# Performance work log

Hardware: AMD Instinct MI355X
Metric: run time of the kernel (lower is better)

The kernel has to match this reference:

```python
import jax, jax.numpy as jnp
import numpy as np

S_LEN, BATCH, HID, HEADS = 2048, 4, 1024, 16
HD = HID // HEADS


def setup_inputs() -> dict:
    key = jax.random.key(0)
    ks = jax.random.split(key, 6)

    def lin_w(k, out_dim, in_dim):
        return jax.random.normal(k, (out_dim, in_dim), jnp.float32) * (1.0 / np.sqrt(in_dim))

    return {
        "hidden_states": jax.random.normal(ks[0], (S_LEN, BATCH, HID), jnp.float32),
        "Wq": lin_w(ks[1], HID, HID), "bq": jnp.zeros((HID,), jnp.float32),
        "Wk": lin_w(ks[2], HID, HID), "bk": jnp.zeros((HID,), jnp.float32),
        "Wv": lin_w(ks[3], HID, HID), "bv": jnp.zeros((HID,), jnp.float32),
        "Wf": lin_w(ks[4], HEADS, HID), "bf": jnp.zeros((HEADS,), jnp.float32),
        "Wo": lin_w(ks[5], HID, HID), "bo": jnp.zeros((HID,), jnp.float32),
    }


def _forget_attention(hidden_states, Wq, bq, Wk, bk, Wv, bv, Wf, bf, Wo, bo):
    S, B, H = hidden_states.shape
    nh, hd = HEADS, HD

    def shape(x):
        return x.reshape(S, B, nh, hd)

    q = shape(hidden_states @ Wq.T + bq)
    k = shape(hidden_states @ Wk.T + bk)
    v = shape(hidden_states @ Wv.T + bv)

    # kernel_fn = elu(x) + 1
    phi_q = jax.nn.elu(q) + 1.0
    phi_k = jax.nn.elu(k) + 1.0

    f = jax.nn.sigmoid(hidden_states @ Wf.T + bf)  # [S, B, nh]

    # F_{t,j} = prod_{i=j+1}^{t} f_i  factorizes into the recurrence:
    #   S_t = f_t * S_{t-1} + phi_k_t (x) v_t ;  z_t = f_t * z_{t-1} + phi_k_t
    # out_t = (phi_q_t . S_t) / (phi_q_t . z_t + eps)
    def step(carry, xs):
        Sm, z = carry                      # [B,nh,hd,hd], [B,nh,hd]
        ft, pk, pq, vt = xs                # [B,nh], [B,nh,hd] x3
        fte = ft[..., None]
        Sm = fte[..., None] * Sm + pk[..., :, None] * vt[..., None, :]
        z = fte * z + pk
        num = jnp.einsum('bhd,bhde->bhe', pq, Sm)
        den = jnp.einsum('bhd,bhd->bh', pq, z)[..., None]
        return (Sm, z), num / (den + 1e-6)

    init = (jnp.zeros((B, nh, hd, hd), hidden_states.dtype),
            jnp.zeros((B, nh, hd), hidden_states.dtype))
    _, out = jax.lax.scan(step, init, (f, phi_k, phi_q, v))

    out = out.reshape(S, B, H) @ Wo.T + bo
    return out, f


def reference(hidden_states, Wq, bq, Wk, bk, Wv, bv, Wf, bf, Wo, bo):
    out, f = _forget_attention(hidden_states, Wq, bq, Wk, bk, Wv, bv, Wf, bf, Wo, bo)
    return (out, jnp.zeros_like(out), f)
```

## Files before the change

### kernel.cpp

```cpp
#include <hip/hip_runtime.h>
#include <hip/hip_bf16.h>
#include <math.h>

#define S_LEN 2048
#define BATCH 4
#define HID   1024
#define HEADS 16
#define HD    64
#define SB    (S_LEN*BATCH)
#define CHUNK 64
#define NCHUNK (S_LEN/CHUNK)
#define BH    (BATCH*HEADS)
#define NSTK  3200

typedef __bf16 bf16x8 __attribute__((ext_vector_type(8)));
typedef float  f32x4  __attribute__((ext_vector_type(4)));
typedef unsigned short ushort_t;
typedef unsigned short u16x8 __attribute__((ext_vector_type(8)));

__device__ __forceinline__ unsigned short f2bf(float x) {
    union { float f; unsigned int u; } un; un.f = x;
    unsigned int u = un.u;
    unsigned int r = (u + 0x7FFFu + ((u >> 16) & 1u)) >> 16;
    return (unsigned short)r;
}
__device__ __forceinline__ float bf2f(unsigned short s) {
    union { unsigned int u; float f; } un; un.u = ((unsigned int)s) << 16;
    return un.f;
}

#define NXU (SB*HID/4)
#define NW1 (NSTK*HID/4)
#define NW2 (HID*HID/4)
#define NBU (NSTK/4)
#define NTOT (NXU+NW1+NW2+NBU)

__global__ __launch_bounds__(256) void prep_kernel(
    const float* __restrict__ X,  const float* __restrict__ Wq,
    const float* __restrict__ Wk, const float* __restrict__ Wv,
    const float* __restrict__ Wf, const float* __restrict__ Wo,
    const float* __restrict__ bq, const float* __restrict__ bk,
    const float* __restrict__ bv, const float* __restrict__ bf,
    ushort_t* __restrict__ Xb, ushort_t* __restrict__ Wstk,
    ushort_t* __restrict__ Wob, float* __restrict__ bstk)
{
    const int i = blockIdx.x * 256 + threadIdx.x;
    if (i < NXU) {
        float4 v = ((const float4*)X)[i];
        ushort4 o; o.x=f2bf(v.x); o.y=f2bf(v.y); o.z=f2bf(v.z); o.w=f2bf(v.w);
        ((ushort4*)Xb)[i] = o;
    } else if (i < NXU + NW1) {
        const int idx4 = (i - NXU) * 4;
        const int row = idx4 >> 10, col = idx4 & 1023;
        float4 v;
        if      (row < 1024) v = *(const float4*)(Wq + (size_t)row*HID + col);
        else if (row < 2048) v = *(const float4*)(Wk + (size_t)(row-1024)*HID + col);
        else if (row < 3072) v = *(const float4*)(Wv + (size_t)(row-2048)*HID + col);
        else if (row < 3088) v = *(const float4*)(Wf + (size_t)(row-3072)*HID + col);
        else                 v = make_float4(0.f,0.f,0.f,0.f);
        ushort4 o; o.x=f2bf(v.x); o.y=f2bf(v.y); o.z=f2bf(v.z); o.w=f2bf(v.w);
        *(ushort4*)(Wstk + idx4) = o;
    } else if (i < NXU + NW1 + NW2) {
        const int idx4 = (i - NXU - NW1) * 4;
        float4 v = *(const float4*)(Wo + idx4);
        ushort4 o; o.x=f2bf(v.x); o.y=f2bf(v.y); o.z=f2bf(v.z); o.w=f2bf(v.w);
        *(ushort4*)(Wob + idx4) = o;
    } else if (i < NTOT) {
        const int idx4 = (i - NXU - NW1 - NW2) * 4;
        #pragma unroll
        for (int t = 0; t < 4; ++t) {
            const int c = idx4 + t;
            float v;
            if      (c < 1024) v = bq[c];
            else if (c < 2048) v = bk[c-1024];
            else if (c < 3072) v = bv[c-2048];
            else if (c < 3088) v = bf[c-3072];
            else               v = 0.f;
            bstk[c] = v;
        }
    }
}

__global__ __launch_bounds__(256) void qkvf_gemm(
    const ushort_t* __restrict__ X, const ushort_t* __restrict__ W,
    const float* __restrict__ bias,
    ushort_t* __restrict__ Q, ushort_t* __restrict__ Kr,
    ushort_t* __restrict__ V,
    float* __restrict__ f_out, float* __restrict__ logf_out)
{
    __shared__ ushort_t As[128 * 32];
    __shared__ ushort_t Bs[128 * 32];

    const int tid  = threadIdx.x;
    const int wave = tid >> 6, lane = tid & 63;
    const int waveM = wave >> 1, waveN = wave & 1;
    const int rowBase = blockIdx.x * 128;
    const int colBase = blockIdx.y * 128;
    const int K = HID;

    f32x4 acc[4][4];
    #pragma unroll
    for (int i = 0; i < 4; ++i)
        #pragma unroll
        for (int j = 0; j < 4; ++j)
            acc[i][j] = (f32x4){0.f, 0.f, 0.f, 0.f};

    const int srow = lane >> 2;
    const int scol = (lane & 3) * 8;

    const ushort_t* gA0 = X + (size_t)(rowBase + wave*16 + srow) * K + scol;
    const ushort_t* gB0 = W + (size_t)(colBase + wave*16 + srow) * K + scol;
    ushort_t* lA = As + (wave*16)*32;
    ushort_t* lB = Bs + (wave*16)*32;

    const int fr = lane & 15;
    const int fk = (lane >> 4) * 8;

    for (int k0 = 0; k0 < K; k0 += 32) {
        __builtin_amdgcn_global_load_lds(
            (const __attribute__((address_space(1))) void*)(gA0 + k0),
            (__attribute__((address_space(3))) void*)lA, 16, 0, 0);
        __builtin_amdgcn_global_load_lds(
            (const __attribute__((address_space(1))) void*)(gA0 + (size_t)64*K + k0),
            (__attribute__((address_space(3))) void*)(lA + 64*32), 16, 0, 0);
        __builtin_amdgcn_global_load_lds(
            (const __attribute__((address_space(1))) void*)(gB0 + k0),
            (__attribute__((address_space(3))) void*)lB, 16, 0, 0);
        __builtin_amdgcn_global_load_lds(
            (const __attribute__((address_space(1))) void*)(gB0 + (size_t)64*K + k0),
            (__attribute__((address_space(3))) void*)(lB + 64*32), 16, 0, 0);

        __syncthreads();

        bf16x8 a[4], b[4];
        #pragma unroll
        for (int i = 0; i < 4; ++i)
            a[i] = *(const bf16x8*)(As + (waveM*64 + i*16 + fr)*32 + fk);
        #pragma unroll
        for (int j = 0; j < 4; ++j)
            b[j] = *(const bf16x8*)(Bs + (waveN*64 + j*16 + fr)*32 + fk);

        #pragma unroll
        for (int i = 0; i < 4; ++i)
            #pragma unroll
            for (int j = 0; j < 4; ++j)
                acc[i][j] = __builtin_amdgcn_mfma_f32_16x16x32_bf16(
                    a[i], b[j], acc[i][j], 0, 0, 0);

        __syncthreads();
    }

    const int er = (lane >> 4) * 4;
    const int ec = lane & 15;
    #pragma unroll
    for (int i = 0; i < 4; ++i) {
        #pragma unroll
        for (int j = 0; j < 4; ++j) {
            const int r0 = rowBase + waveM*64 + i*16 + er;
            const int c0 = colBase + waveN*64 + j*16;
            if (c0 >= 3088) continue;
            const int c  = c0 + ec;
            const float bv = bias[c];
            #pragma unroll
            for (int k = 0; k < 4; ++k) {
                float v = acc[i][j][k] + bv;
                const int r = r0 + k;
                if (c0 < 1024) {
                    v = (v > 0.f) ? (v + 1.f) : __expf(v);
                    Q[(size_t)r * HID + c] = f2bf(v);
                } else if (c0 < 2048) {
                    v = (v > 0.f) ? (v + 1.f) : __expf(v);
                    Kr[(size_t)r * HID + (c - 1024)] = f2bf(v);
                } else if (c0 < 3072) {
                    V[(size_t)r * HID + (c - 2048)] = f2bf(v);
                } else {
                    const int n = c - 3072;
                    const float fv = 1.f / (1.f + __expf(-v));
                    f_out[(size_t)r * HEADS + n]    = fv;
                    logf_out[(size_t)r * HEADS + n] = -__logf(1.f + __expf(-v));
                }
            }
        }
    }
}

__global__ __launch_bounds__(256) void gemm_out(
    const ushort_t* __restrict__ X, const ushort_t* __restrict__ W,
    const float* __restrict__ bias, float* __restrict__ Y,
    float* __restrict__ Yzero)
{
    __shared__ ushort_t As[128 * 32];
    __shared__ ushort_t Bs[128 * 32];

    const int tid  = threadIdx.x;
    const int wave = tid >> 6, lane = tid & 63;
    const int waveM = wave >> 1, waveN = wave & 1;
    const int rowBase = blockIdx.x * 128;
    const int colBase = blockIdx.y * 128;
    const int K = HID, N = HID;

    f32x4 acc[4][4];
    #pragma unroll
    for (int i = 0; i < 4; ++i)
        #pragma unroll
        for (int j = 0; j < 4; ++j)
            acc[i][j] = (f32x4){0.f, 0.f, 0.f, 0.f};

    const int srow = lane >> 2;
    const int scol = (lane & 3) * 8;

    const ushort_t* gA0 = X + (size_t)(rowBase + wave*16 + srow) * K + scol;
    const ushort_t* gB0 = W + (size_t)(colBase + wave*16 + srow) * K + scol;
    ushort_t* lA = As + (wave*16)*32;
    ushort_t* lB = Bs + (wave*16)*32;

    const int fr = lane & 15;
    const int fk = (lane >> 4) * 8;

    for (int k0 = 0; k0 < K; k0 += 32) {
        __builtin_amdgcn_global_load_lds(
            (const __attribute__((address_space(1))) void*)(gA0 + k0),
            (__attribute__((address_space(3))) void*)lA, 16, 0, 0);
        __builtin_amdgcn_global_load_lds(
            (const __attribute__((address_space(1))) void*)(gA0 + (size_t)64*K + k0),
            (__attribute__((address_space(3))) void*)(lA + 64*32), 16, 0, 0);
        __builtin_amdgcn_global_load_lds(
            (const __attribute__((address_space(1))) void*)(gB0 + k0),
            (__attribute__((address_space(3))) void*)lB, 16, 0, 0);
        __builtin_amdgcn_global_load_lds(
            (const __attribute__((address_space(1))) void*)(gB0 + (size_t)64*K + k0),
            (__attribute__((address_space(3))) void*)(lB + 64*32), 16, 0, 0);

        __syncthreads();

        bf16x8 a[4], b[4];
        #pragma unroll
        for (int i = 0; i < 4; ++i)
            a[i] = *(const bf16x8*)(As + (waveM*64 + i*16 + fr)*32 + fk);
        #pragma unroll
        for (int j = 0; j < 4; ++j)
            b[j] = *(const bf16x8*)(Bs + (waveN*64 + j*16 + fr)*32 + fk);

        #pragma unroll
        for (int i = 0; i < 4; ++i)
            #pragma unroll
            for (int j = 0; j < 4; ++j)
                acc[i][j] = __builtin_amdgcn_mfma_f32_16x16x32_bf16(
                    a[i], b[j], acc[i][j], 0, 0, 0);

        __syncthreads();
    }

    const int er = (lane >> 4) * 4;
    const int ec = lane & 15;
    #pragma unroll
    for (int i = 0; i < 4; ++i) {
        #pragma unroll
        for (int j = 0; j < 4; ++j) {
            const int r0 = rowBase + waveM*64 + i*16 + er;
            const int c  = colBase + waveN*64 + j*16 + ec;
            const float bv = bias[c];
            #pragma unroll
            for (int k = 0; k < 4; ++k) {
                const size_t off = (size_t)(r0 + k) * N + c;
                Y[off] = acc[i][j][k] + bv;
                Yzero[off] = 0.f;
            }
        }
    }
}

__global__ __launch_bounds__(256) void pass1_kernel(
    const ushort_t* __restrict__ Kp, const ushort_t* __restrict__ Vp,
    const float* __restrict__ logf,
    float* __restrict__ Schunk, float* __restrict__ zchunk,
    float* __restrict__ Dchunk)
{
    __shared__ __align__(16) char smem[18688];
    ushort_t* vsT = (ushort_t*)smem;
    ushort_t* kTd = (ushort_t*)(smem + 9216);
    float*    exd = (float*)(smem + 18432);

    const int chunk = blockIdx.x;
    const int bh = blockIdx.y;
    const int b = bh >> 4, h = bh & 15;
    const int tid = threadIdx.x;
    const int wv = tid >> 6, ln = tid & 63;
    const int fr = ln & 15, q4 = ln >> 4;
    const size_t slot = (size_t)bh * NCHUNK + chunk;

    u16x8 vreg[2], kreg[2];
    #pragma unroll
    for (int it = 0; it < 2; ++it) {
        const int u = it*256 + tid;
        const int j = u >> 3, d8 = (u & 7) * 8;
        const size_t base = (size_t)((chunk*64 + j)*BATCH + b)*HID + h*HD + d8;
        vreg[it] = *(const u16x8*)(Vp + base);
        kreg[it] = *(const u16x8*)(Kp + base);
    }
    if (tid < 64) {
        float v = logf[(size_t)((chunk*64 + tid)*BATCH + b) * HEADS + h];
        #pragma unroll
        for (int off = 1; off < 64; off <<= 1) {
            float n = __shfl_up(v, off);
            if (tid >= off) v += n;
        }
        const float tot = __shfl(v, 63);
        exd[tid] = __expf(tot - v);
        if (tid == 63) Dchunk[slot] = __expf(tot);
    }
    __syncthreads();

    #pragma unroll
    for (int it = 0; it < 2; ++it) {
        const int u = it*256 + tid;
        const int j = u >> 3, d8 = (u & 7) * 8;
        const float ex = exd[j];
        #pragma unroll
        for (int i = 0; i < 8; ++i) {
            vsT[(d8+i)*72 + j] = vreg[it][i];
            kTd[(d8+i)*72 + j] = f2bf(bf2f(kreg[it][i]) * ex);
        }
    }
    __syncthreads();

    f32x4 acc[4];
    #pragma unroll
    for (int nt = 0; nt < 4; ++nt) acc[nt] = (f32x4){0.f,0.f,0.f,0.f};
    #pragma unroll
    for (int k0 = 0; k0 < 64; k0 += 32) {
        bf16x8 av = *(const bf16x8*)(vsT + (wv*16 + fr)*72 + k0 + q4*8);
        #pragma unroll
        for (int nt = 0; nt < 4; ++nt) {
            bf16x8 bk = *(const bf16x8*)(kTd + (nt*16 + fr)*72 + k0 + q4*8);
            acc[nt] = __builtin_amdgcn_mfma_f32_16x16x32_bf16(av, bk, acc[nt], 0, 0, 0);
        }
    }

    if (wv == 0) {
        u16x8 onesu;
        #pragma unroll
        for (int i = 0; i < 8; ++i) onesu[i] = 0x3F80;
        const bf16x8 ones = *(const bf16x8*)&onesu;
        f32x4 zacc[4];
        #pragma unroll
        for (int nt = 0; nt < 4; ++nt) zacc[nt] = (f32x4){0.f,0.f,0.f,0.f};
        #pragma unroll
        for (int k0 = 0; k0 < 64; k0 += 32) {
            #pragma unroll
            for (int nt = 0; nt < 4; ++nt) {
                bf16x8 bk = *(const bf16x8*)(kTd + (nt*16 + fr)*72 + k0 + q4*8);
                zacc[nt] = __builtin_amdgcn_mfma_f32_16x16x32_bf16(ones, bk, zacc[nt], 0, 0, 0);
            }
        }
        if (q4 == 0) {
            #pragma unroll
            for (int nt = 0; nt < 4; ++nt)
                zchunk[slot*64 + nt*16 + fr] = zacc[nt][0];
        }
    }

    float* sp = Schunk + slot * 4096;
    #pragma unroll
    for (int nt = 0; nt < 4; ++nt) {
        #pragma unroll
        for (int r = 0; r < 4; ++r) {
            const int e = wv*16 + q4*4 + r;
            sp[e*64 + nt*16 + fr] = acc[nt][r];
        }
    }
}

__global__ __launch_bounds__(256) void pass2_kernel(
    float* __restrict__ Schunk, float* __restrict__ zchunk,
    const float* __restrict__ Dchunk)
{
    const int bh = blockIdx.x;
    const int tid = threadIdx.x;

    float Sprev[16];
    #pragma unroll
    for (int i = 0; i < 16; ++i) Sprev[i] = 0.f;
    float zprev = 0.f;

    const size_t base  = (size_t)bh * NCHUNK * 4096;
    const size_t zbase = (size_t)bh * NCHUNK * 64;

    for (int c = 0; c < NCHUNK; ++c) {
        const float D = Dchunk[bh * NCHUNK + c];
        float* sp = Schunk + base + (size_t)c * 4096;
        float contrib[16];
        #pragma unroll
        for (int i = 0; i < 16; ++i) contrib[i] = sp[i*256 + tid];
        #pragma unroll
        for (int i = 0; i < 16; ++i) {
            sp[i*256 + tid] = Sprev[i];
            Sprev[i] = D * Sprev[i] + contrib[i];
        }
        if (tid < 64) {
            float* zp = zchunk + zbase + (size_t)c * 64;
            const float zc = zp[tid];
            zp[tid] = zprev;
            zprev = D * zprev + zc;
        }
    }
}

__global__ __launch_bounds__(256) void pass3_kernel(
    const ushort_t* __restrict__ Qp, const ushort_t* __restrict__ Kp,
    const ushort_t* __restrict__ Vp, const float* __restrict__ logf,
    const float* __restrict__ S0, const float* __restrict__ z0,
    ushort_t* __restrict__ AO)
{
    __shared__ __align__(16) char smem[28672];
    ushort_t* qs  = (ushort_t*)smem;
    ushort_t* ks  = (ushort_t*)(smem + 9216);
    ushort_t* vsT = (ushort_t*)(smem + 9216);
    ushort_t* psA = (ushort_t*)(smem + 18432);
    float* cc  = (float*)(smem + 27648);
    float* exT = (float*)(smem + 27904);
    float* qz  = (float*)(smem + 28160);
    float* den = (float*)(smem + 28416);

    const int chunk = blockIdx.x;
    const int bh = blockIdx.y;
    const int b = bh >> 4, h = bh & 15;
    const int tid = threadIdx.x;
    const int wv = tid >> 6, ln = tid & 63;
    const int fr = ln & 15, q4 = ln >> 4;
    const size_t slot = (size_t)bh * NCHUNK + chunk;

    u16x8 vreg[2];
    #pragma unroll
    for (int it = 0; it < 2; ++it) {
        const int u = it*256 + tid;
        const int j = u >> 3, d8 = (u & 7) * 8;
        vreg[it] = *(const u16x8*)(Vp + (size_t)((chunk*64 + j)*BATCH + b)*HID + h*HD + d8);
    }

    if (tid < 64) {
        float v = logf[(size_t)((chunk*64 + tid)*BATCH + b) * HEADS + h];
        #pragma unroll
        for (int off = 1; off < 64; off <<= 1) {
            float n = __shfl_up(v, off);
            if (tid >= off) v += n;
        }
        cc[tid]  = v;
        exT[tid] = __expf(v);
    }
    #pragma unroll
    for (int it = 0; it < 2; ++it) {
        const int u = it*256 + tid;
        const int r = u >> 3, c8 = (u & 7) * 8;
        const size_t goff = (size_t)((chunk*64 + r)*BATCH + b) * HID + h*HD + c8;
        *(u16x8*)(qs + r*72 + c8) = *(const u16x8*)(Qp + goff);
        *(u16x8*)(ks + r*72 + c8) = *(const u16x8*)(Kp + goff);
    }
    __syncthreads();

    f32x4 pacc[4];
    #pragma unroll
    for (int nt = 0; nt < 4; ++nt) pacc[nt] = (f32x4){0.f,0.f,0.f,0.f};
    #pragma unroll
    for (int k0 = 0; k0 < 64; k0 += 32) {
        bf16x8 af = *(const bf16x8*)(qs + (wv*16 + fr)*72 + k0 + q4*8);
        #pragma unroll
        for (int nt = 0; nt < 4; ++nt) {
            bf16x8 bfr = *(const bf16x8*)(ks + (nt*16 + fr)*72 + k0 + q4*8);
            pacc[nt] = __builtin_amdgcn_mfma_f32_16x16x32_bf16(af, bfr, pacc[nt], 0, 0, 0);
        }
    }
    if (tid < 64) {
        float zown = z0[slot * 64 + tid];
        float s = 0.f;
        for (int d = 0; d < 64; ++d) {
            const float zd = __shfl(zown, d);
            s += bf2f(qs[tid*72 + d]) * zd;
        }
        qz[tid] = s;
    }
    __syncthreads();

    #pragma unroll
    for (int it = 0; it < 2; ++it) {
        const int u = it*256 + tid;
        const int j = u >> 3, d8 = (u & 7) * 8;
        #pragma unroll
        for (int i = 0; i < 8; ++i)
            vsT[(d8+i)*72 + j] = vreg[it][i];
    }
    {
        float rs[4] = {0.f, 0.f, 0.f, 0.f};
        float cct[4];
        #pragma unroll
        for (int r = 0; r < 4; ++r) cct[r] = cc[wv*16 + q4*4 + r];
        #pragma unroll
        for (int nt = 0; nt < 4; ++nt) {
            const int j = nt*16 + fr;
            const float ccj = cc[j];
            #pragma unroll
            for (int r = 0; r < 4; ++r) {
                const int t = wv*16 + q4*4 + r;
                float p = (j <= t) ? pacc[nt][r] * __expf(cct[r] - ccj) : 0.f;
                rs[r] += p;
                psA[t*72 + j] = f2bf(p);
            }
        }
        #pragma unroll
        for (int m = 1; m < 16; m <<= 1) {
            #pragma unroll
            for (int r = 0; r < 4; ++r) rs[r] += __shfl_xor(rs[r], m);
        }
        if (fr == 0) {
            #pragma unroll
            for (int r = 0; r < 4; ++r) {
                const int t = wv*16 + q4*4 + r;
                den[t] = rs[r] + exT[t] * qz[t] + 1e-6f;
            }
        }
    }
    __syncthreads();

    f32x4 oacc[4], oacc2[4];
    #pragma unroll
    for (int nt = 0; nt < 4; ++nt) {
        oacc[nt]  = (f32x4){0.f,0.f,0.f,0.f};
        oacc2[nt] = (f32x4){0.f,0.f,0.f,0.f};
    }
    const float* S0p = S0 + slot * 4096;
    #pragma unroll
    for (int k0 = 0; k0 < 64; k0 += 32) {
        const int k8 = k0 + q4*8;
        bf16x8 ap = *(const bf16x8*)(psA + (wv*16 + fr)*72 + k8);
        bf16x8 aq = *(const bf16x8*)(qs  + (wv*16 + fr)*72 + k8);
        #pragma unroll
        for (int nt = 0; nt < 4; ++nt) {
            bf16x8 bv = *(const bf16x8*)(vsT + (nt*16 + fr)*72 + k8);
            oacc[nt] = __builtin_amdgcn_mfma_f32_16x16x32_bf16(ap, bv, oacc[nt], 0, 0, 0);
            f32x4 s0a = *(const f32x4*)(S0p + (nt*16 + fr)*64 + k8);
            f32x4 s0b = *(const f32x4*)(S0p + (nt*16 + fr)*64 + k8 + 4);
            u16x8 sb;
            #pragma unroll
            for (int i = 0; i < 4; ++i) { sb[i] = f2bf(s0a[i]); sb[4+i] = f2bf(s0b[i]); }
            oacc2[nt] = __builtin_amdgcn_mfma_f32_16x16x32_bf16(aq, *(bf16x8*)&sb, oacc2[nt], 0, 0, 0);
        }
    }
    #pragma unroll
    for (int nt = 0; nt < 4; ++nt) {
        const int e = nt*16 + fr;
        #pragma unroll
        for (int r = 0; r < 4; ++r) {
            const int t = wv*16 + q4*4 + r;
            const float v = (oacc[nt][r] + exT[t] * oacc2[nt][r]) / den[t];
            AO[(size_t)((chunk*64 + t)*BATCH + b) * HID + h*HD + e] = f2bf(v);
        }
    }
}

extern "C" void kernel_launch(void* const* d_in, const int* in_sizes, int n_in,
                              void* d_out, int out_size, void* d_ws, size_t ws_size,
                              hipStream_t stream) {
    const float* X  = (const float*)d_in[0];
    const float* Wq = (const float*)d_in[1];
    const float* bq = (const float*)d_in[2];
    const float* Wk = (const float*)d_in[3];
    const float* bk = (const float*)d_in[4];
    const float* Wv = (const float*)d_in[5];
    const float* bv = (const float*)d_in[6];
    const float* Wf = (const float*)d_in[7];
    const float* bf = (const float*)d_in[8];
    const float* Wo = (const float*)d_in[9];
    const float* bo = (const float*)d_in[10];

    float* out = (float*)d_out;
    const size_t OUT_SLOT = (size_t)SB * HID;

    char* ws = (char*)d_ws;
    ushort_t* wsXb   = (ushort_t*)ws;
    ushort_t* wsWstk = wsXb + (size_t)SB * HID;
    ushort_t* wsWob  = wsWstk + (size_t)NSTK * HID;
    ushort_t* wsQ    = wsWob + (size_t)HID * HID;
    ushort_t* wsK    = wsQ + (size_t)SB * HID;
    ushort_t* wsV    = wsK + (size_t)SB * HID;
    float* wsBstk = (float*)(wsV + (size_t)SB * HID);
    float* wsLogf = wsBstk + NSTK;
    float* wsS    = wsLogf + (size_t)SB * HEADS;
    float* wsZ    = wsS + (size_t)BH * NCHUNK * HD * HD;
    float* wsD    = wsZ + (size_t)BH * NCHUNK * HD;

    prep_kernel<<<(NTOT + 255)/256, 256, 0, stream>>>(
        X, Wq, Wk, Wv, Wf, Wo, bq, bk, bv, bf,
        wsXb, wsWstk, wsWob, wsBstk);

    dim3 qgrid(SB/128, NSTK/128);
    qkvf_gemm<<<qgrid, 256, 0, stream>>>(
        wsXb, wsWstk, wsBstk, wsQ, wsK, wsV,
        out + 2*OUT_SLOT, wsLogf);

    dim3 sgrid(NCHUNK, BH);
    pass1_kernel<<<sgrid, 256, 0, stream>>>(wsK, wsV, wsLogf, wsS, wsZ, wsD);
    pass2_kernel<<<BH, 256, 0, stream>>>(wsS, wsZ, wsD);
    pass3_kernel<<<sgrid, 256, 0, stream>>>(wsQ, wsK, wsV, wsLogf, wsS, wsZ, wsXb);

    dim3 ogrid(SB/128, HID/128);
    gemm_out<<<ogrid, 256, 0, stream>>>(wsXb, wsWob, bo, out, out + OUT_SLOT);
}
```

Before: 300.8 us.

## Use 32x32 MFMA in GEMMs, store chunk states in bf16, prefetch in scan

Both GEMM kernels switch from 16x16x32 to 32x32x16 bf16 MFMA tiles, with the epilogue indexing remapped to match. The per-chunk state matrices are now stored in bf16 rather than fp32, which halves their traffic across pass1, pass2 and pass3. Pass2 software-prefetches the next two chunks' states into registers to hide load latency in its serial loop. Pass3 computes the q·z dot product across all waves with shuffles instead of a serial 64-step loop. Storing the carried state in bf16 adds rounding error to the inter-chunk prefix.

```diff
diff --git a/kernel.cpp b/kernel.cpp
--- a/kernel.cpp
+++ b/kernel.cpp
@@ -15,6 +15,7 @@
 
 typedef __bf16 bf16x8 __attribute__((ext_vector_type(8)));
 typedef float  f32x4  __attribute__((ext_vector_type(4)));
+typedef float  f32x16 __attribute__((ext_vector_type(16)));
 typedef unsigned short ushort_t;
 typedef unsigned short u16x8 __attribute__((ext_vector_type(8)));
 
@@ -98,12 +99,12 @@
     const int colBase = blockIdx.y * 128;
     const int K = HID;
 
-    f32x4 acc[4][4];
-    #pragma unroll
-    for (int i = 0; i < 4; ++i)
-        #pragma unroll
-        for (int j = 0; j < 4; ++j)
-            acc[i][j] = (f32x4){0.f, 0.f, 0.f, 0.f};
+    f32x16 acc[2][2];
+    #pragma unroll
+    for (int i = 0; i < 2; ++i)
+        #pragma unroll
+        for (int j = 0; j < 2; ++j)
+            acc[i][j] = (f32x16){};
 
     const int srow = lane >> 2;
     const int scol = (lane & 3) * 8;
@@ -113,8 +114,8 @@
     ushort_t* lA = As + (wave*16)*32;
     ushort_t* lB = Bs + (wave*16)*32;
 
-    const int fr = lane & 15;
-    const int fk = (lane >> 4) * 8;
+    const int m32 = lane & 31;
+    const int kh  = (lane >> 5) * 8;
 
     for (int k0 = 0; k0 < K; k0 += 32) {
         __builtin_amdgcn_global_load_lds(
@@ -132,52 +133,54 @@
 
         __syncthreads();
 
-        bf16x8 a[4], b[4];
-        #pragma unroll
-        for (int i = 0; i < 4; ++i)
-            a[i] = *(const bf16x8*)(As + (waveM*64 + i*16 + fr)*32 + fk);
-        #pragma unroll
-        for (int j = 0; j < 4; ++j)
-            b[j] = *(const bf16x8*)(Bs + (waveN*64 + j*16 + fr)*32 + fk);
-
-        #pragma unroll
-        for (int i = 0; i < 4; ++i)
-            #pragma unroll
-            for (int j = 0; j < 4; ++j)
-                acc[i][j] = __builtin_amdgcn_mfma_f32_16x16x32_bf16(
-                    a[i], b[j], acc[i][j], 0, 0, 0);
+        bf16x8 a[2][2], b[2][2];
+        #pragma unroll
+        for (int sm = 0; sm < 2; ++sm)
+            #pragma unroll
+            for (int ks = 0; ks < 2; ++ks) {
+                a[sm][ks] = *(const bf16x8*)(As + (waveM*64 + sm*32 + m32)*32 + ks*16 + kh);
+                b[sm][ks] = *(const bf16x8*)(Bs + (waveN*64 + sm*32 + m32)*32 + ks*16 + kh);
+            }
+
+        #pragma unroll
+        for (int ks = 0; ks < 2; ++ks)
+            #pragma unroll
+            for (int sm = 0; sm < 2; ++sm)
+                #pragma unroll
+                for (int sn = 0; sn < 2; ++sn)
+                    acc[sm][sn] = __builtin_amdgcn_mfma_f32_32x32x16_bf16(
+                        a[sm][ks], b[sn][ks], acc[sm][sn], 0, 0, 0);
 
         __syncthreads();
     }
 
-    const int er = (lane >> 4) * 4;
-    const int ec = lane & 15;
-    #pragma unroll
-    for (int i = 0; i < 4; ++i) {
-        #pragma unroll
-        for (int j = 0; j < 4; ++j) {
-            const int r0 = rowBase + waveM*64 + i*16 + er;
-            const int c0 = colBase + waveN*64 + j*16;
+    const int c32 = lane & 31;
+    const int r4  = (lane >> 5) * 4;
+    #pragma unroll
+    for (int sm = 0; sm < 2; ++sm) {
+        #pragma unroll
+        for (int sn = 0; sn < 2; ++sn) {
+            const int c0 = colBase + waveN*64 + sn*32;
             if (c0 >= 3088) continue;
-            const int c  = c0 + ec;
+            const int c  = c0 + c32;
             const float bv = bias[c];
             #pragma unroll
-            for (int k = 0; k < 4; ++k) {
-                float v = acc[i][j][k] + bv;
-                const int r = r0 + k;
+            for (int reg = 0; reg < 16; ++reg) {
+                const int row = rowBase + waveM*64 + sm*32
+                              + (reg & 3) + ((reg >> 2) * 8) + r4;
+                float v = acc[sm][sn][reg] + bv;
                 if (c0 < 1024) {
                     v = (v > 0.f) ? (v + 1.f) : __expf(v);
-                    Q[(size_t)r * HID + c] = f2bf(v);
+                    Q[(size_t)row * HID + c] = f2bf(v);
                 } else if (c0 < 2048) {
                     v = (v > 0.f) ? (v + 1.f) : __expf(v);
-                    Kr[(size_t)r * HID + (c - 1024)] = f2bf(v);
+                    Kr[(size_t)row * HID + (c - 1024)] = f2bf(v);
                 } else if (c0 < 3072) {
-                    V[(size_t)r * HID + (c - 2048)] = f2bf(v);
-                } else {
-                    const int n = c - 3072;
+                    V[(size_t)row * HID + (c - 2048)] = f2bf(v);
+                } else if (c32 < 16) {
                     const float fv = 1.f / (1.f + __expf(-v));
-                    f_out[(size_t)r * HEADS + n]    = fv;
-                    logf_out[(size_t)r * HEADS + n] = -__logf(1.f + __expf(-v));
+                    f_out[(size_t)row * HEADS + (c - 3072)]    = fv;
+                    logf_out[(size_t)row * HEADS + (c - 3072)] = -__logf(1.f + __expf(-v));
                 }
             }
         }
@@ -199,12 +202,12 @@
     const int colBase = blockIdx.y * 128;
     const int K = HID, N = HID;
 
-    f32x4 acc[4][4];
-    #pragma unroll
-    for (int i = 0; i < 4; ++i)
-        #pragma unroll
-        for (int j = 0; j < 4; ++j)
-            acc[i][j] = (f32x4){0.f, 0.f, 0.f, 0.f};
+    f32x16 acc[2][2];
+    #pragma unroll
+    for (int i = 0; i < 2; ++i)
+        #pragma unroll
+        for (int j = 0; j < 2; ++j)
+            acc[i][j] = (f32x16){};
 
     const int srow = lane >> 2;
     const int scol = (lane & 3) * 8;
@@ -214,8 +217,8 @@
     ushort_t* lA = As + (wave*16)*32;
     ushort_t* lB = Bs + (wave*16)*32;
 
-    const int fr = lane & 15;
-    const int fk = (lane >> 4) * 8;
+    const int m32 = lane & 31;
+    const int kh  = (lane >> 5) * 8;
 
     for (int k0 = 0; k0 < K; k0 += 32) {
         __builtin_amdgcn_global_load_lds(
@@ -233,37 +236,41 @@
 
         __syncthreads();
 
-        bf16x8 a[4], b[4];
-        #pragma unroll
-        for (int i = 0; i < 4; ++i)
-            a[i] = *(const bf16x8*)(As + (waveM*64 + i*16 + fr)*32 + fk);
-        #pragma unroll
-        for (int j = 0; j < 4; ++j)
-            b[j] = *(const bf16x8*)(Bs + (waveN*64 + j*16 + fr)*32 + fk);
-
-        #pragma unroll
-        for (int i = 0; i < 4; ++i)
-            #pragma unroll
-            for (int j = 0; j < 4; ++j)
-                acc[i][j] = __builtin_amdgcn_mfma_f32_16x16x32_bf16(
-                    a[i], b[j], acc[i][j], 0, 0, 0);
+        bf16x8 a[2][2], b[2][2];
+        #pragma unroll
+        for (int sm = 0; sm < 2; ++sm)
+            #pragma unroll
+            for (int ks = 0; ks < 2; ++ks) {
+                a[sm][ks] = *(const bf16x8*)(As + (waveM*64 + sm*32 + m32)*32 + ks*16 + kh);
+                b[sm][ks] = *(const bf16x8*)(Bs + (waveN*64 + sm*32 + m32)*32 + ks*16 + kh);
+            }
+
+        #pragma unroll
+        for (int ks = 0; ks < 2; ++ks)
+            #pragma unroll
+            for (int sm = 0; sm < 2; ++sm)
+                #pragma unroll
+                for (int sn = 0; sn < 2; ++sn)
+                    acc[sm][sn] = __builtin_amdgcn_mfma_f32_32x32x16_bf16(
+                        a[sm][ks], b[sn][ks], acc[sm][sn], 0, 0, 0);
 
         __syncthreads();
     }
 
-    const int er = (lane >> 4) * 4;
-    const int ec = lane & 15;
-    #pragma unroll
-    for (int i = 0; i < 4; ++i) {
-        #pragma unroll
-        for (int j = 0; j < 4; ++j) {
-            const int r0 = rowBase + waveM*64 + i*16 + er;
-            const int c  = colBase + waveN*64 + j*16 + ec;
+    const int c32 = lane & 31;
+    const int r4  = (lane >> 5) * 4;
+    #pragma unroll
+    for (int sm = 0; sm < 2; ++sm) {
+        #pragma unroll
+        for (int sn = 0; sn < 2; ++sn) {
+            const int c = colBase + waveN*64 + sn*32 + c32;
             const float bv = bias[c];
             #pragma unroll
-            for (int k = 0; k < 4; ++k) {
-                const size_t off = (size_t)(r0 + k) * N + c;
-                Y[off] = acc[i][j][k] + bv;
+            for (int reg = 0; reg < 16; ++reg) {
+                const int row = rowBase + waveM*64 + sm*32
+                              + (reg & 3) + ((reg >> 2) * 8) + r4;
+                const size_t off = (size_t)row * N + c;
+                Y[off] = acc[sm][sn][reg] + bv;
                 Yzero[off] = 0.f;
             }
         }
@@ -273,7 +280,7 @@
 __global__ __launch_bounds__(256) void pass1_kernel(
     const ushort_t* __restrict__ Kp, const ushort_t* __restrict__ Vp,
     const float* __restrict__ logf,
-    float* __restrict__ Schunk, float* __restrict__ zchunk,
+    ushort_t* __restrict__ Schunk, float* __restrict__ zchunk,
     float* __restrict__ Dchunk)
 {
     __shared__ __align__(16) char smem[18688];
@@ -360,19 +367,19 @@
         }
     }
 
-    float* sp = Schunk + slot * 4096;
+    ushort_t* sp = Schunk + slot * 4096;
     #pragma unroll
     for (int nt = 0; nt < 4; ++nt) {
         #pragma unroll
         for (int r = 0; r < 4; ++r) {
             const int e = wv*16 + q4*4 + r;
-            sp[e*64 + nt*16 + fr] = acc[nt][r];
+            sp[e*64 + nt*16 + fr] = f2bf(acc[nt][r]);
         }
     }
 }
 
 __global__ __launch_bounds__(256) void pass2_kernel(
-    float* __restrict__ Schunk, float* __restrict__ zchunk,
+    ushort_t* __restrict__ Schunk, float* __restrict__ zchunk,
     const float* __restrict__ Dchunk)
 {
     const int bh = blockIdx.x;
@@ -386,22 +393,39 @@
     const size_t base  = (size_t)bh * NCHUNK * 4096;
     const size_t zbase = (size_t)bh * NCHUNK * 64;
 
+    ushort_t b0[16], b1[16];
+    float z0v = 0.f, z1v = 0.f;
+    #pragma unroll
+    for (int i = 0; i < 16; ++i) {
+        b0[i] = Schunk[base + 0*4096 + i*256 + tid];
+        b1[i] = Schunk[base + 1*4096 + i*256 + tid];
+    }
+    if (tid < 64) {
+        z0v = zchunk[zbase + 0*64 + tid];
+        z1v = zchunk[zbase + 1*64 + tid];
+    }
+
     for (int c = 0; c < NCHUNK; ++c) {
         const float D = Dchunk[bh * NCHUNK + c];
-        float* sp = Schunk + base + (size_t)c * 4096;
-        float contrib[16];
-        #pragma unroll
-        for (int i = 0; i < 16; ++i) contrib[i] = sp[i*256 + tid];
+        ushort_t* sp = Schunk + base + (size_t)c * 4096;
         #pragma unroll
         for (int i = 0; i < 16; ++i) {
-            sp[i*256 + tid] = Sprev[i];
-            Sprev[i] = D * Sprev[i] + contrib[i];
+            const float contrib = bf2f(b0[i]);
+            sp[i*256 + tid] = f2bf(Sprev[i]);
+            Sprev[i] = D * Sprev[i] + contrib;
+            b0[i] = b1[i];
         }
         if (tid < 64) {
-            float* zp = zchunk + zbase + (size_t)c * 64;
-            const float zc = zp[tid];
-            zp[tid] = zprev;
+            const float zc = z0v;
+            zchunk[zbase + (size_t)c * 64 + tid] = zprev;
             zprev = D * zprev + zc;
+            z0v = z1v;
+        }
+        if (c + 2 < NCHUNK) {
+            #pragma unroll
+            for (int i = 0; i < 16; ++i)
+                b1[i] = Schunk[base + (size_t)(c+2)*4096 + i*256 + tid];
+            if (tid < 64) z1v = zchunk[zbase + (size_t)(c+2)*64 + tid];
         }
     }
 }
@@ -409,10 +433,10 @@
 __global__ __launch_bounds__(256) void pass3_kernel(
     const ushort_t* __restrict__ Qp, const ushort_t* __restrict__ Kp,
     const ushort_t* __restrict__ Vp, const float* __restrict__ logf,
-    const float* __restrict__ S0, const float* __restrict__ z0,
+    const ushort_t* __restrict__ S0, const float* __restrict__ z0,
     ushort_t* __restrict__ AO)
 {
-    __shared__ __align__(16) char smem[28672];
+    __shared__ __align__(16) char smem[28928];
     ushort_t* qs  = (ushort_t*)smem;
     ushort_t* ks  = (ushort_t*)(smem + 9216);
     ushort_t* vsT = (ushort_t*)(smem + 9216);
@@ -421,6 +445,7 @@
     float* exT = (float*)(smem + 27904);
     float* qz  = (float*)(smem + 28160);
     float* den = (float*)(smem + 28416);
+    float* zz  = (float*)(smem + 28672);
 
     const int chunk = blockIdx.x;
     const int bh = blockIdx.y;
@@ -439,6 +464,7 @@
     }
 
     if (tid < 64) {
+        zz[tid] = z0[slot * 64 + tid];
         float v = logf[(size_t)((chunk*64 + tid)*BATCH + b) * HEADS + h];
         #pragma unroll
         for (int off = 1; off < 64; off <<= 1) {
@@ -470,14 +496,16 @@
             pacc[nt] = __builtin_amdgcn_mfma_f32_16x16x32_bf16(af, bfr, pacc[nt], 0, 0, 0);
         }
     }
-    if (tid < 64) {
-        float zown = z0[slot * 64 + tid];
+    {
+        const int t = wv*16 + fr;
+        const int d0 = q4 * 16;
         float s = 0.f;
-        for (int d = 0; d < 64; ++d) {
-            const float zd = __shfl(zown, d);
-            s += bf2f(qs[tid*72 + d]) * zd;
-        }
-        qz[tid] = s;
+        #pragma unroll
+        for (int i = 0; i < 16; ++i)
+            s += bf2f(qs[t*72 + d0 + i]) * zz[d0 + i];
+        s += __shfl_xor(s, 16);
+        s += __shfl_xor(s, 32);
+        if (q4 == 0) qz[t] = s;
     }
     __syncthreads();
 
@@ -527,7 +555,7 @@
         oacc[nt]  = (f32x4){0.f,0.f,0.f,0.f};
         oacc2[nt] = (f32x4){0.f,0.f,0.f,0.f};
     }
-    const float* S0p = S0 + slot * 4096;
+    const ushort_t* S0p = S0 + slot * 4096;
     #pragma unroll
     for (int k0 = 0; k0 < 64; k0 += 32) {
         const int k8 = k0 + q4*8;
@@ -537,12 +565,8 @@
         for (int nt = 0; nt < 4; ++nt) {
             bf16x8 bv = *(const bf16x8*)(vsT + (nt*16 + fr)*72 + k8);
             oacc[nt] = __builtin_amdgcn_mfma_f32_16x16x32_bf16(ap, bv, oacc[nt], 0, 0, 0);
-            f32x4 s0a = *(const f32x4*)(S0p + (nt*16 + fr)*64 + k8);
-            f32x4 s0b = *(const f32x4*)(S0p + (nt*16 + fr)*64 + k8 + 4);
-            u16x8 sb;
-            #pragma unroll
-            for (int i = 0; i < 4; ++i) { sb[i] = f2bf(s0a[i]); sb[4+i] = f2bf(s0b[i]); }
-            oacc2[nt] = __builtin_amdgcn_mfma_f32_16x16x32_bf16(aq, *(bf16x8*)&sb, oacc2[nt], 0, 0, 0);
+            bf16x8 sb = *(const bf16x8*)(S0p + (nt*16 + fr)*64 + k8);
+            oacc2[nt] = __builtin_amdgcn_mfma_f32_16x16x32_bf16(aq, sb, oacc2[nt], 0, 0, 0);
         }
     }
     #pragma unroll
@@ -584,8 +608,8 @@
     ushort_t* wsV    = wsK + (size_t)SB * HID;
     float* wsBstk = (float*)(wsV + (size_t)SB * HID);
     float* wsLogf = wsBstk + NSTK;
-    float* wsS    = wsLogf + (size_t)SB * HEADS;
-    float* wsZ    = wsS + (size_t)BH * NCHUNK * HD * HD;
+    ushort_t* wsS  = (ushort_t*)(wsLogf + (size_t)SB * HEADS);
+    float* wsZ    = (float*)(wsS + (size_t)BH * NCHUNK * HD * HD);
     float* wsD    = wsZ + (size_t)BH * NCHUNK * HD;
 
     prep_kernel<<<(NTOT + 255)/256, 256, 0, stream>>>(
```

Result: no change. 304.8 us (+1.3%).
